# Kernel optimization log

Measured on AMD Instinct MI355X. Metric: run time of the kernel, lower is better.

The kernel has to match this reference:

```python
import jax, jax.numpy as jnp
import numpy as np
from jax import lax

EPS = 1e-5
DW_THR = 4.0    # threshold for depthwise-branch channel pruning
PW_THR = 0.001  # threshold for pointwise-branch channel pruning


def _bn(x, gamma, beta, mean, var):
    # inference-mode BatchNorm2d over channel dim (NCHW)
    inv = gamma / jnp.sqrt(var + EPS)
    return x * inv[None, :, None, None] + (beta - mean * inv)[None, :, None, None]


def _prune(x, thr):
    # zero every (batch, channel) slice whose max abs value is < thr
    keep = jnp.max(jnp.abs(x), axis=(2, 3), keepdims=True) >= thr  # [B,C,1,1]
    return x * lax.stop_gradient(keep).astype(x.dtype)


def setup_inputs() -> dict:
    key = jax.random.key(0)
    ks = jax.random.split(key, 12)
    B, C, O, H, W = 64, 128, 256, 56, 56
    x = jax.random.normal(ks[0], (B, C, H, W), jnp.float32)
    dw_w = jax.random.normal(ks[1], (C, 1, 3, 3), jnp.float32) * 0.2   # depthwise OIHW, groups=C
    dw_b = jax.random.normal(ks[2], (C,), jnp.float32) * 0.1
    g1 = 1.0 + 0.2 * jax.random.normal(ks[3], (C,), jnp.float32)
    b1 = 0.1 * jax.random.normal(ks[4], (C,), jnp.float32)
    m1 = 0.1 * jax.random.normal(ks[5], (C,), jnp.float32)
    v1 = jax.random.uniform(ks[6], (C,), jnp.float32, 0.5, 1.5)
    pw_w = jax.random.normal(ks[7], (O, C, 1, 1), jnp.float32) * (1.0 / np.sqrt(C))
    pw_b = jax.random.normal(ks[8], (O,), jnp.float32) * 0.1
    g2 = 1.0 + 0.2 * jax.random.normal(ks[9], (O,), jnp.float32)
    b2 = 0.1 * jax.random.normal(ks[10], (O,), jnp.float32)
    m2 = 0.1 * jax.random.normal(ks[11], (O,), jnp.float32)
    v2 = jnp.ones((O,), jnp.float32)
    return {"x": x, "dw_w": dw_w, "dw_b": dw_b, "g1": g1, "b1": b1, "m1": m1, "v1": v1,
            "pw_w": pw_w, "pw_b": pw_b, "g2": g2, "b2": b2, "m2": m2, "v2": v2}


def reference(x, dw_w, dw_b, g1, b1, m1, v1, pw_w, pw_b, g2, b2, m2, v2):
    C = dw_w.shape[0]
    # depthwise 3x3 conv, padding=1, groups=C
    y = lax.conv_general_dilated(
        x, dw_w, window_strides=(1, 1), padding=[(1, 1), (1, 1)],
        dimension_numbers=("NCHW", "OIHW", "NCHW"), feature_group_count=C)
    y = y + dw_b[None, :, None, None]
    y = jax.nn.relu(_bn(y, g1, b1, m1, v1))
    y = _prune(y, DW_THR)
    # pointwise 1x1 conv
    z = jnp.einsum("bchw,oc->bohw", y, pw_w[:, :, 0, 0]) + pw_b[None, :, None, None]
    z = jax.nn.relu(_bn(z, g2, b2, m2, v2))
    z = _prune(z, PW_THR)
    return z
```

## Files before the change

### kernel.cpp

```cpp
#include <hip/hip_runtime.h>
#include <stdint.h>

#define EPSV 1e-5f

typedef __attribute__((ext_vector_type(8))) short short8;
typedef __attribute__((ext_vector_type(4))) float floatx4;

__device__ __forceinline__ unsigned short f2bf(float f) {
    union { float f; uint32_t u; } v; v.f = f;
    uint32_t u = v.u;
    return (unsigned short)((u + 0x7FFFu + ((u >> 16) & 1u)) >> 16);
}

__global__ __launch_bounds__(256) void k_fold(
        const float* __restrict__ pw_w, const float* __restrict__ pw_b,
        const float* __restrict__ g2, const float* __restrict__ b2,
        const float* __restrict__ m2, const float* __restrict__ v2,
        unsigned short* __restrict__ w_bf, float* __restrict__ bias2) {
    int idx = blockIdx.x * 256 + threadIdx.x;
    int o = idx >> 7, c = idx & 127;
    float inv = g2[o] / sqrtf(v2[o] + EPSV);
    w_bf[idx] = f2bf(pw_w[idx] * inv);
    if (c == 0) bias2[o] = pw_b[o] * inv + b2[o] - m2[o] * inv;
}

__global__ __launch_bounds__(256) void k_dw(
        const float* __restrict__ x, const float* __restrict__ dw_w,
        const float* __restrict__ dw_b, const float* __restrict__ g1,
        const float* __restrict__ b1, const float* __restrict__ m1,
        const float* __restrict__ v1, unsigned short* __restrict__ y_ws) {
    const int c = blockIdx.x, b = blockIdx.y;
    const int t = threadIdx.x;
    __shared__ float halo[58 * 58];
    __shared__ float red[4];

    const float* xs = x + (size_t)(b * 128 + c) * 3136;
    for (int i = t; i < 3364; i += 256) {
        int r = i / 58, cc = i - r * 58;
        int gh = r - 1, gw = cc - 1;
        float v = 0.f;
        if ((unsigned)gh < 56u && (unsigned)gw < 56u) v = xs[gh * 56 + gw];
        halo[i] = v;
    }
    const float* wk = dw_w + c * 9;
    float k0 = wk[0], k1 = wk[1], k2 = wk[2], k3 = wk[3], k4 = wk[4],
          k5 = wk[5], k6 = wk[6], k7 = wk[7], k8 = wk[8];
    float inv1 = g1[c] / sqrtf(v1[c] + EPSV);
    float add0 = dw_b[c] * inv1 + b1[c] - m1[c] * inv1;
    __syncthreads();

    float yv[14];
    float mx = 0.f;
    #pragma unroll
    for (int i = 0; i < 7; ++i) {
        int base = i * 512 + 2 * t;
        if (base < 3136) {
            int h = base / 56, w = base - h * 56;
            const float* r0 = &halo[h * 58 + w];
            const float* r1 = r0 + 58;
            const float* r2 = r1 + 58;
            float a0 = r0[0], a1 = r0[1], a2 = r0[2], a3 = r0[3];
            float b0 = r1[0], b1_ = r1[1], b2_ = r1[2], b3 = r1[3];
            float c0 = r2[0], c1 = r2[1], c2 = r2[2], c3 = r2[3];
            float s0 = k0*a0 + k1*a1 + k2*a2 + k3*b0 + k4*b1_ + k5*b2_ + k6*c0 + k7*c1 + k8*c2;
            float s1 = k0*a1 + k1*a2 + k2*a3 + k3*b1_ + k4*b2_ + k5*b3 + k6*c1 + k7*c2 + k8*c3;
            float y0 = fmaxf(s0 * inv1 + add0, 0.f);
            float y1 = fmaxf(s1 * inv1 + add0, 0.f);
            mx = fmaxf(mx, fmaxf(y0, y1));
            yv[2 * i] = y0; yv[2 * i + 1] = y1;
        }
    }
    #pragma unroll
    for (int off = 32; off; off >>= 1) mx = fmaxf(mx, __shfl_xor(mx, off));
    if ((t & 63) == 0) red[t >> 6] = mx;
    __syncthreads();
    float m4 = fmaxf(fmaxf(red[0], red[1]), fmaxf(red[2], red[3]));
    float scale = (m4 >= 4.0f) ? 1.f : 0.f;

    uint32_t* yo = (uint32_t*)(y_ws + (size_t)(b * 128 + c) * 3136);
    #pragma unroll
    for (int i = 0; i < 7; ++i) {
        int base = i * 512 + 2 * t;
        if (base < 3136) {
            unsigned short h0 = f2bf(yv[2 * i] * scale);
            unsigned short h1 = f2bf(yv[2 * i + 1] * scale);
            yo[base >> 1] = (uint32_t)h0 | ((uint32_t)h1 << 16);
        }
    }
}

__global__ __launch_bounds__(256) void k_pw(
        const unsigned short* __restrict__ y_ws,
        const unsigned short* __restrict__ w_bf,
        const float* __restrict__ bias2, float* __restrict__ z) {
    const int nt = blockIdx.x;
    const int mt = blockIdx.y;
    const int b  = blockIdx.z;
    const int t = threadIdx.x;
    __shared__ __align__(16) short A_s[128 * 128];
    __shared__ __align__(16) short B_s[128 * 128];

    {
        const uint4* src = (const uint4*)(w_bf + mt * 128 * 128);
        uint4* dst = (uint4*)A_s;
        #pragma unroll
        for (int i = 0; i < 8; ++i) dst[i * 256 + t] = src[i * 256 + t];
    }
    {
        int n0 = nt * 128;
        int crow = t >> 4;
        int nch = (t & 15) * 8;
        #pragma unroll
        for (int i = 0; i < 8; ++i) {
            int c = crow + i * 16;
            int n = n0 + nch;
            uint4 v = make_uint4(0, 0, 0, 0);
            if (n < 3136)
                v = *(const uint4*)(y_ws + (size_t)(b * 128 + c) * 3136 + n);
            *(uint4*)&B_s[c * 128 + nch] = v;
        }
    }
    __syncthreads();

    const int wv = t >> 6, lane = t & 63;
    const int wm = wv >> 1, wn = wv & 1;
    const int q = lane >> 4, r = lane & 15;

    floatx4 acc[4][4];
    #pragma unroll
    for (int i = 0; i < 4; ++i)
        #pragma unroll
        for (int j = 0; j < 4; ++j) acc[i][j] = (floatx4)0.f;

    #pragma unroll
    for (int kk = 0; kk < 4; ++kk) {
        short8 a[4], bb[4];
        #pragma unroll
        for (int it = 0; it < 4; ++it)
            a[it] = *(const short8*)&A_s[(wm * 64 + it * 16 + r) * 128 + kk * 32 + q * 8];
        #pragma unroll
        for (int jt = 0; jt < 4; ++jt) {
            short8 tmp;
            #pragma unroll
            for (int e = 0; e < 8; ++e)
                tmp[e] = B_s[(kk * 32 + q * 8 + e) * 128 + wn * 64 + jt * 16 + r];
            bb[jt] = tmp;
        }
        #pragma unroll
        for (int it = 0; it < 4; ++it)
            #pragma unroll
            for (int jt = 0; jt < 4; ++jt)
                acc[it][jt] = __builtin_amdgcn_mfma_f32_16x16x32_bf16(
                    a[it], bb[jt], acc[it][jt], 0, 0, 0);
    }

    const int n_base = nt * 128 + wn * 64;
    const int o_base = mt * 128 + wm * 64;
    float* zb = z + (size_t)b * 256 * 3136;
    #pragma unroll
    for (int it = 0; it < 4; ++it) {
        int o0 = o_base + it * 16 + q * 4;
        floatx4 bias = *(const floatx4*)(bias2 + o0);
        #pragma unroll
        for (int jt = 0; jt < 4; ++jt) {
            int n = n_base + jt * 16 + r;
            if (n < 3136) {
                #pragma unroll
                for (int j = 0; j < 4; ++j) {
                    float vz = fmaxf(acc[it][jt][j] + bias[j], 0.f);
                    zb[(size_t)(o0 + j) * 3136 + n] = vz;
                }
            }
        }
    }
}

extern "C" void kernel_launch(void* const* d_in, const int* in_sizes, int n_in,
                              void* d_out, int out_size, void* d_ws, size_t ws_size,
                              hipStream_t stream) {
    const float* x    = (const float*)d_in[0];
    const float* dw_w = (const float*)d_in[1];
    const float* dw_b = (const float*)d_in[2];
    const float* g1   = (const float*)d_in[3];
    const float* b1   = (const float*)d_in[4];
    const float* m1   = (const float*)d_in[5];
    const float* v1   = (const float*)d_in[6];
    const float* pw_w = (const float*)d_in[7];
    const float* pw_b = (const float*)d_in[8];
    const float* g2   = (const float*)d_in[9];
    const float* b2   = (const float*)d_in[10];
    const float* m2   = (const float*)d_in[11];
    const float* v2   = (const float*)d_in[12];
    float* z = (float*)d_out;

    unsigned short* y_ws = (unsigned short*)d_ws;
    unsigned short* w_bf = (unsigned short*)((char*)d_ws + 51380224);
    float* bias2         = (float*)((char*)d_ws + 51380224 + 65536);

    hipLaunchKernelGGL(k_fold, dim3(128), dim3(256), 0, stream,
                       pw_w, pw_b, g2, b2, m2, v2, w_bf, bias2);
    hipLaunchKernelGGL(k_dw, dim3(128, 64), dim3(256), 0, stream,
                       x, dw_w, dw_b, g1, b1, m1, v1, y_ws);
    hipLaunchKernelGGL(k_pw, dim3(25, 2, 64), dim3(256), 0, stream,
                       y_ws, w_bf, bias2, z);
}
```

Baseline: 368.6 us.

## Compute all 256 outputs per block with weights in registers and swizzled transposed B tile

The pointwise GEMM block now covers all 256 output channels, so each activation tile is loaded once instead of twice. Each wave loads its 64-row weight slice straight from global memory into registers, which drops the shared-memory A tile. The activation tile is stored transposed in shared memory with an XOR swizzle, so B fragments become single 16-byte reads instead of eight scalar LDS reads. The cost is heavier register use (128 accumulator floats plus 64 weight registers, with launch bounds raised to 2 blocks per CU) and scalar 2-byte transposing stores into LDS.

Result: faster. 359.0 us (-2.6%).

```diff
diff --git a/kernel.cpp b/kernel.cpp
--- a/kernel.cpp
+++ b/kernel.cpp
@@ -89,80 +89,75 @@
     }
 }
 
-__global__ __launch_bounds__(256) void k_pw(
-        const unsigned short* __restrict__ y_ws,
+__global__ __launch_bounds__(256, 2) void k_pw(
+        const unsigned short* __restrict__ y,
         const unsigned short* __restrict__ w_bf,
         const float* __restrict__ bias2, float* __restrict__ z) {
     const int nt = blockIdx.x;
-    const int mt = blockIdx.y;
-    const int b  = blockIdx.z;
+    const int b  = blockIdx.y;
     const int t = threadIdx.x;
-    __shared__ __align__(16) short A_s[128 * 128];
+    const int w = t >> 6, lane = t & 63;
+    const int q = lane >> 4, r = lane & 15;
     __shared__ __align__(16) short B_s[128 * 128];
 
+    short8 a[4][4];
+    #pragma unroll
+    for (int it = 0; it < 4; ++it)
+        #pragma unroll
+        for (int kk = 0; kk < 4; ++kk)
+            a[it][kk] = *(const short8*)(w_bf +
+                (size_t)(w * 64 + it * 16 + r) * 128 + kk * 32 + q * 8);
+
     {
-        const uint4* src = (const uint4*)(w_bf + mt * 128 * 128);
-        uint4* dst = (uint4*)A_s;
-        #pragma unroll
-        for (int i = 0; i < 8; ++i) dst[i * 256 + t] = src[i * 256 + t];
-    }
-    {
-        int n0 = nt * 128;
-        int crow = t >> 4;
-        int nch = (t & 15) * 8;
+        const int n0 = nt * 128;
+        const int nch = (t & 15) * 8;
+        const int sw = (t & 7) << 4;
         #pragma unroll
         for (int i = 0; i < 8; ++i) {
-            int c = crow + i * 16;
-            int n = n0 + nch;
+            int c = (t >> 4) + i * 16;
+            int cp = c ^ sw;
             uint4 v = make_uint4(0, 0, 0, 0);
-            if (n < 3136)
-                v = *(const uint4*)(y_ws + (size_t)(b * 128 + c) * 3136 + n);
-            *(uint4*)&B_s[c * 128 + nch] = v;
+            if (n0 + nch < 3136)
+                v = *(const uint4*)(y + (size_t)(b * 128 + c) * 3136 + n0 + nch);
+            const short* sv = (const short*)&v;
+            #pragma unroll
+            for (int j = 0; j < 8; ++j)
+                B_s[(nch + j) * 128 + cp] = sv[j];
         }
     }
     __syncthreads();
 
-    const int wv = t >> 6, lane = t & 63;
-    const int wm = wv >> 1, wn = wv & 1;
-    const int q = lane >> 4, r = lane & 15;
-
-    floatx4 acc[4][4];
+    floatx4 acc[4][8];
     #pragma unroll
     for (int i = 0; i < 4; ++i)
         #pragma unroll
-        for (int j = 0; j < 4; ++j) acc[i][j] = (floatx4)0.f;
+        for (int j = 0; j < 8; ++j) acc[i][j] = (floatx4)0.f;
 
     #pragma unroll
     for (int kk = 0; kk < 4; ++kk) {
-        short8 a[4], bb[4];
-        #pragma unroll
-        for (int it = 0; it < 4; ++it)
-            a[it] = *(const short8*)&A_s[(wm * 64 + it * 16 + r) * 128 + kk * 32 + q * 8];
-        #pragma unroll
-        for (int jt = 0; jt < 4; ++jt) {
-            short8 tmp;
-            #pragma unroll
-            for (int e = 0; e < 8; ++e)
-                tmp[e] = B_s[(kk * 32 + q * 8 + e) * 128 + wn * 64 + jt * 16 + r];
-            bb[jt] = tmp;
+        short8 bb[8];
+        #pragma unroll
+        for (int jt = 0; jt < 8; ++jt) {
+            int nl = jt * 16 + r;
+            int cs = (kk * 32 + q * 8) ^ ((((nl >> 3) & 7)) << 4);
+            bb[jt] = *(const short8*)&B_s[nl * 128 + cs];
         }
         #pragma unroll
         for (int it = 0; it < 4; ++it)
             #pragma unroll
-            for (int jt = 0; jt < 4; ++jt)
+            for (int jt = 0; jt < 8; ++jt)
                 acc[it][jt] = __builtin_amdgcn_mfma_f32_16x16x32_bf16(
-                    a[it], bb[jt], acc[it][jt], 0, 0, 0);
-    }
-
-    const int n_base = nt * 128 + wn * 64;
-    const int o_base = mt * 128 + wm * 64;
+                    a[it][kk], bb[jt], acc[it][jt], 0, 0, 0);
+    }
+
+    const int n_base = nt * 128;
     float* zb = z + (size_t)b * 256 * 3136;
     #pragma unroll
     for (int it = 0; it < 4; ++it) {
-        int o0 = o_base + it * 16 + q * 4;
+        int o0 = w * 64 + it * 16 + q * 4;
         floatx4 bias = *(const floatx4*)(bias2 + o0);
         #pragma unroll
-        for (int jt = 0; jt < 4; ++jt) {
+        for (int jt = 0; jt < 8; ++jt) {
             int n = n_base + jt * 16 + r;
             if (n < 3136) {
                 #pragma unroll
@@ -193,14 +188,15 @@
     const float* v2   = (const float*)d_in[12];
     float* z = (float*)d_out;
 
+    const size_t YB = 51380224;
     unsigned short* y_ws = (unsigned short*)d_ws;
-    unsigned short* w_bf = (unsigned short*)((char*)d_ws + 51380224);
-    float* bias2         = (float*)((char*)d_ws + 51380224 + 65536);
+    unsigned short* w_bf = (unsigned short*)((char*)d_ws + YB);
+    float* bias2         = (float*)((char*)d_ws + YB + 65536);
 
     hipLaunchKernelGGL(k_fold, dim3(128), dim3(256), 0, stream,
                        pw_w, pw_b, g2, b2, m2, v2, w_bf, bias2);
     hipLaunchKernelGGL(k_dw, dim3(128, 64), dim3(256), 0, stream,
                        x, dw_w, dw_b, g1, b1, m1, v1, y_ws);
-    hipLaunchKernelGGL(k_pw, dim3(25, 2, 64), dim3(256), 0, stream,
+    hipLaunchKernelGGL(k_pw, dim3(25, 64), dim3(256), 0, stream,
                        y_ws, w_bf, bias2, z);
 }
```
